# Performance work log

Measured on AMD Instinct MI355X. Metric: run time of the kernel, lower is better.

## Reference

```python
import jax, jax.numpy as jnp
import numpy as np

V, E, H = 50000, 300, 512
B, S = 64, 512


def setup_inputs() -> dict:
    key = jax.random.key(0)
    ks = jax.random.split(key, 10)
    sc = 1.0 / np.sqrt(H)
    return {
        "inputs": jax.random.randint(ks[0], (B, S), 0, V),
        "embed_table": jax.random.normal(ks[1], (V, E), jnp.float32),
        "W_ih_f": jax.random.normal(ks[2], (4 * H, E), jnp.float32) * sc,
        "W_hh_f": jax.random.normal(ks[3], (4 * H, H), jnp.float32) * sc,
        "b_ih_f": jax.random.normal(ks[4], (4 * H,), jnp.float32) * sc,
        "b_hh_f": jax.random.normal(ks[5], (4 * H,), jnp.float32) * sc,
        "W_ih_b": jax.random.normal(ks[6], (4 * H, E), jnp.float32) * sc,
        "W_hh_b": jax.random.normal(ks[7], (4 * H, H), jnp.float32) * sc,
        "b_ih_b": jax.random.normal(ks[8], (4 * H,), jnp.float32) * sc,
        "b_hh_b": jax.random.normal(ks[9], (4 * H,), jnp.float32) * sc,
    }


def _cell_from_gates(gates):
    # PyTorch LSTMCell gate order: i, f, g, o; here c_prev == 0 (faithful to source bug)
    i, f, g, o = jnp.split(gates, 4, axis=-1)
    c = jax.nn.sigmoid(i) * jnp.tanh(g)
    return jax.nn.sigmoid(o) * jnp.tanh(c)


def reference(inputs, embed_table, W_ih_f, W_hh_f, b_ih_f, b_hh_f,
              W_ih_b, W_hh_b, b_ih_b, b_hh_b):
    x = embed_table[inputs]  # [B,S,E]
    # 'forward LSTM': source always feeds (zero, zero) state -> no recurrence,
    # fully parallel over time. h contribution from W_hh is zero.
    gates_f = jnp.einsum('bse,ge->bsg', x, W_ih_f) + b_ih_f + b_hh_f  # [B,S,4H]
    h_f = _cell_from_gates(gates_f)  # [B,S,H]

    # backward LSTM: h carried across steps, c_prev always zero (faithful)
    x_gates_b = jnp.einsum('bse,ge->bsg', x, W_ih_b) + b_ih_b + b_hh_b  # [B,S,4H]
    xs = jnp.flip(x_gates_b, axis=1).transpose(1, 0, 2)  # [S,B,4H] reversed time

    def step(h, xt):
        h_new = _cell_from_gates(xt + h @ W_hh_b.T)
        return h_new, h_new

    h0 = jnp.zeros((x.shape[0], W_hh_b.shape[1]), x.dtype)
    _, hs_b = jax.lax.scan(step, h0, xs)  # [S,B,H], reversed time order
    h_b = jnp.flip(hs_b.transpose(1, 0, 2), axis=1)  # [B,S,H] original order

    concat = jnp.concatenate([h_f, h_b], axis=-1)  # [B,S,2H]
    return jnp.max(concat, axis=1)  # [B,2H]
```

## Files before the change

kernel.cpp:

```cpp
#include <hip/hip_runtime.h>
#include <cstdint>
#include <cstddef>

#define B_   64
#define S_   512
#define E_   300
#define EP   320
#define H_   512
#define G3   1536
#define CHUNKS 8
#define CHLEN  64
#define HALO   32
#define WPG    8

typedef float  f32x4 __attribute__((ext_vector_type(4)));
typedef short  s16x8 __attribute__((ext_vector_type(8)));
typedef unsigned long long u64;

__device__ __forceinline__ unsigned short f2bf(float f) {
  union { float f; unsigned u; } v; v.f = f;
  return (unsigned short)((v.u + 0x7fffu + ((v.u >> 16) & 1u)) >> 16);
}
__device__ __forceinline__ float bf2f(unsigned short s) {
  union { unsigned u; float f; } v; v.u = ((unsigned)s) << 16;
  return v.f;
}
__device__ __forceinline__ float sigm(float x) { return 1.0f / (1.0f + __expf(-x)); }
__device__ __forceinline__ float tanhf_(float x) { return 2.0f / (1.0f + __expf(-2.0f * x)) - 1.0f; }
__device__ __forceinline__ float cellh(float i, float g, float o) {
  float c = sigm(i) * tanhf_(g);
  return sigm(o) * tanhf_(c);
}

__device__ __forceinline__ float ldG(const float* p, long i) { return p[i]; }
__device__ __forceinline__ float ldG(const unsigned short* p, long i) { return bf2f(p[i]); }
__device__ __forceinline__ void stG(float* p, long i, float v) { p[i] = v; }
__device__ __forceinline__ void stG(unsigned short* p, long i, float v) { p[i] = f2bf(v); }
__device__ __forceinline__ void ld2G(const float* p, long i, float& a, float& b) {
  float2 t = *(const float2*)(p + i); a = t.x; b = t.y;
}
__device__ __forceinline__ void ld2G(const unsigned short* p, long i, float& a, float& b) {
  unsigned u = *(const unsigned*)(p + i);
  a = bf2f((unsigned short)(u & 0xffffu)); b = bf2f((unsigned short)(u >> 16));
}
__device__ __forceinline__ void ld4G(const float* p, long i, float4& v) {
  v = *(const float4*)(p + i);
}
__device__ __forceinline__ void ld4G(const unsigned short* p, long i, float4& v) {
  u64 u = *(const u64*)(p + i);
  v.x = bf2f((unsigned short)(u & 0xffffu));
  v.y = bf2f((unsigned short)((u >> 16) & 0xffffu));
  v.z = bf2f((unsigned short)((u >> 32) & 0xffffu));
  v.w = bf2f((unsigned short)(u >> 48));
}

__device__ __forceinline__ void bar_lgkm() {
  asm volatile("s_waitcnt lgkmcnt(0)\ns_barrier" ::: "memory");
}
__device__ __forceinline__ void bar_only() {
  asm volatile("s_barrier" ::: "memory");
}

__global__ __launch_bounds__(256)
void prep_kernel(const float* __restrict__ Wf, const float* __restrict__ Wb,
                 const float* __restrict__ bihf, const float* __restrict__ bhhf,
                 const float* __restrict__ bihb, const float* __restrict__ bhhb,
                 unsigned short* __restrict__ Wfp, unsigned short* __restrict__ Wbp,
                 float* __restrict__ bpf, float* __restrict__ bpb) {
  const int t0 = blockIdx.x * blockDim.x + threadIdx.x;
  const int stride = gridDim.x * blockDim.x;
  const int tot = G3 * EP;
  for (int idx = t0; idx < tot; idx += stride) {
    const int n = idx / EP, k = idx - n * EP;
    const int src = (n < H_) ? n : n + H_;
    const float vf = (k < E_) ? Wf[(size_t)src * E_ + k] : 0.0f;
    const float vb = (k < E_) ? Wb[(size_t)src * E_ + k] : 0.0f;
    Wfp[idx] = f2bf(vf);
    Wbp[idx] = f2bf(vb);
  }
  for (int n = t0; n < G3; n += stride) {
    const int src = (n < H_) ? n : n + H_;
    bpf[n] = bihf[src] + bhhf[src];
    bpb[n] = bihb[src] + bhhb[src];
  }
}

__global__ __launch_bounds__(256)
void xstage_kernel(const int* __restrict__ inp, const float* __restrict__ emb,
                   unsigned short* __restrict__ xbf) {
  const int t = blockIdx.x * blockDim.x + threadIdx.x;
  const int row = t / 80, q = t - row * 80;
  const int c0 = q * 4;
  const int vid = inp[row];
  unsigned short o[4];
#pragma unroll
  for (int e = 0; e < 4; ++e) {
    const int c = c0 + e;
    o[e] = (c < E_) ? f2bf(emb[(size_t)vid * E_ + c]) : (unsigned short)0;
  }
  uint2 pv;
  pv.x = (unsigned)o[0] | ((unsigned)o[1] << 16);
  pv.y = (unsigned)o[2] | ((unsigned)o[3] << 16);
  *(uint2*)&xbf[(size_t)row * EP + c0] = pv;
}

template<bool REMAP, typename GT>
__global__ __launch_bounds__(256)
void gemm_kernel(const unsigned short* __restrict__ A, const unsigned short* __restrict__ W,
                 const float* __restrict__ bias, GT* __restrict__ C) {
  __shared__ short lA[128 * 40];
  __shared__ short lB[128 * 40];
  const int tid = threadIdx.x;
  const int w = tid >> 6, l = tid & 63;
  const int wr = w >> 1, wc = w & 1;
  const int Mb = blockIdx.x * 128, Nb = blockIdx.y * 128;
  f32x4 acc[4][4];
#pragma unroll
  for (int i = 0; i < 4; ++i)
#pragma unroll
    for (int j = 0; j < 4; ++j) acc[i][j] = f32x4{0.f, 0.f, 0.f, 0.f};

  const int srow = tid >> 1, shalf = (tid & 1) * 16;
  for (int kk = 0; kk < EP; kk += 32) {
    const s16x8* ga = (const s16x8*)&A[(size_t)(Mb + srow) * EP + kk + shalf];
    const s16x8* gb = (const s16x8*)&W[(size_t)(Nb + srow) * EP + kk + shalf];
    s16x8 a0 = ga[0], a1 = ga[1], b0 = gb[0], b1 = gb[1];
    *(s16x8*)&lA[srow * 40 + shalf]     = a0;
    *(s16x8*)&lA[srow * 40 + shalf + 8] = a1;
    *(s16x8*)&lB[srow * 40 + shalf]     = b0;
    *(s16x8*)&lB[srow * 40 + shalf + 8] = b1;
    __syncthreads();
    s16x8 af[4], bf[4];
#pragma unroll
    for (int mt = 0; mt < 4; ++mt)
      af[mt] = *(const s16x8*)&lA[(wr * 64 + mt * 16 + (l & 15)) * 40 + 8 * (l >> 4)];
#pragma unroll
    for (int nt = 0; nt < 4; ++nt)
      bf[nt] = *(const s16x8*)&lB[(wc * 64 + nt * 16 + (l & 15)) * 40 + 8 * (l >> 4)];
#pragma unroll
    for (int mt = 0; mt < 4; ++mt)
#pragma unroll
      for (int nt = 0; nt < 4; ++nt)
        acc[mt][nt] = __builtin_amdgcn_mfma_f32_16x16x32_bf16(af[mt], bf[nt], acc[mt][nt], 0, 0, 0);
    __syncthreads();
  }
#pragma unroll
  for (int mt = 0; mt < 4; ++mt) {
#pragma unroll
    for (int nt = 0; nt < 4; ++nt) {
      const int gc = Nb + wc * 64 + nt * 16 + (l & 15);
      const float bv = bias[gc];
#pragma unroll
      for (int r = 0; r < 4; ++r) {
        const int gr = Mb + wr * 64 + mt * 16 + (l >> 4) * 4 + r;
        const int orow = REMAP ? (((gr & 511) << 6) | (gr >> 9)) : gr;
        stG(C, (long)orow * G3 + gc, acc[mt][nt][r] + bv);
      }
    }
  }
}

template<typename GT>
__global__ __launch_bounds__(256)
void cellmax1_kernel(const GT* __restrict__ G, float* __restrict__ part) {
  const int b = blockIdx.x, ch = blockIdx.y, tid = threadIdx.x;
  const int j0 = tid * 2;
  float mx0 = -2.f, mx1 = -2.f;
#pragma unroll 1
  for (int s = ch * 64; s < ch * 64 + 64; ++s) {
    const long base = (long)(b * S_ + s) * G3;
    float i0, i1, g0, g1, o0, o1;
    ld2G(G, base + j0, i0, i1);
    ld2G(G, base + 512 + j0, g0, g1);
    ld2G(G, base + 1024 + j0, o0, o1);
    mx0 = fmaxf(mx0, cellh(i0, g0, o0));
    mx1 = fmaxf(mx1, cellh(i1, g1, o1));
  }
  part[(ch * 64 + b) * 512 + j0]     = mx0;
  part[(ch * 64 + b) * 512 + j0 + 1] = mx1;
}

__global__ __launch_bounds__(256)
void cellmax2_kernel(const float* __restrict__ part, float* __restrict__ out) {
  const int b = blockIdx.x, tid = threadIdx.x;
  const int j0 = tid * 2;
  float mx0 = -2.f, mx1 = -2.f;
#pragma unroll
  for (int ch = 0; ch < 8; ++ch) {
    const float2 v = *(const float2*)&part[(ch * 64 + b) * 512 + j0];
    mx0 = fmaxf(mx0, v.x);
    mx1 = fmaxf(mx1, v.y);
  }
  out[b * 1024 + j0] = mx0;
  out[b * 1024 + j0 + 1] = mx1;
}

__global__ __launch_bounds__(256)
void breduce_kernel(const float* __restrict__ bpart, float* __restrict__ out) {
  const int b = blockIdx.x, tid = threadIdx.x;
  const int j0 = tid * 2;
  float mx0 = -2.f, mx1 = -2.f;
#pragma unroll
  for (int ch = 0; ch < CHUNKS; ++ch) {
    const float2 v = *(const float2*)&bpart[(ch * 64 + b) * 512 + j0];
    mx0 = fmaxf(mx0, v.x);
    mx1 = fmaxf(mx1, v.y);
  }
  out[b * 1024 + 512 + j0] = mx0;
  out[b * 1024 + 512 + j0 + 1] = mx1;
}

__global__ __launch_bounds__(256) void zero_sync_kernel(unsigned* p) {
  for (int i = threadIdx.x; i < 4096; i += 256) p[i] = 0;
}

template<typename GT>
__global__ __launch_bounds__(384, 1)
void scan_kernel(const float* __restrict__ Whh, const GT* __restrict__ Gb,
                 u64* __restrict__ hbuf, unsigned* __restrict__ flags,
                 float* __restrict__ bpart) {
  __shared__ __align__(16) unsigned hl[16 * 262];
  __shared__ float gbuf[12][16][20];

  const int tid = threadIdx.x;
  const int wv = tid >> 6, l = tid & 63;
  const int grp = blockIdx.x >> 3, rank = blockIdx.x & 7;
  const int ch = blockIdx.y;
  const int dom = grp * CHUNKS + ch;
  const int jbase = rank * 64;

  const int own_lo = ch * CHLEN, own_hi = own_lo + CHLEN;
  int ts = own_hi - 1 + HALO;
  if (ts > S_ - 1) ts = S_ - 1;

  const int tt0 = wv * 2, tt1 = tt0 + 1;
  s16x8 wf0[16], wf1[16];
  {
    const int nb0 = (tt0 >> 2) * 512 + jbase + (tt0 & 3) * 16 + (l & 15);
    const int nb1 = (tt1 >> 2) * 512 + jbase + (tt1 & 3) * 16 + (l & 15);
    const int s0 = (nb0 < 512) ? nb0 : nb0 + 512;
    const int s1 = (nb1 < 512) ? nb1 : nb1 + 512;
    const float* w0 = Whh + (size_t)s0 * 512 + 8 * (l >> 4);
    const float* w1 = Whh + (size_t)s1 * 512 + 8 * (l >> 4);
#pragma unroll
    for (int kc = 0; kc < 16; ++kc) {
      float4 a = *(const float4*)(w0 + kc * 32);
      float4 b = *(const float4*)(w0 + kc * 32 + 4);
      s16x8 v;
      v[0] = (short)f2bf(a.x); v[1] = (short)f2bf(a.y);
      v[2] = (short)f2bf(a.z); v[3] = (short)f2bf(a.w);
      v[4] = (short)f2bf(b.x); v[5] = (short)f2bf(b.y);
      v[6] = (short)f2bf(b.z); v[7] = (short)f2bf(b.w);
      wf0[kc] = v;
      a = *(const float4*)(w1 + kc * 32);
      b = *(const float4*)(w1 + kc * 32 + 4);
      v[0] = (short)f2bf(a.x); v[1] = (short)f2bf(a.y);
      v[2] = (short)f2bf(a.z); v[3] = (short)f2bf(a.w);
      v[4] = (short)f2bf(b.x); v[5] = (short)f2bf(b.y);
      v[6] = (short)f2bf(b.z); v[7] = (short)f2bf(b.w);
      wf1[kc] = v;
    }
  }

  const int mrow = (l >> 4) * 4;
  const int slot = tid - 64;
  const bool nl  = (slot >= 0 && slot < 256);
  const int prow = nl ? (slot >> 4) : 0;
  const int q    = slot & 15;
  const int tile = q >> 2, cit0 = (q & 3) * 4;
  const unsigned short* hls = (const unsigned short*)hl;
  float4 mx = {-2.f, -2.f, -2.f, -2.f};

  float4 xi = {0,0,0,0}, xg = {0,0,0,0}, xo = {0,0,0,0};
  if (nl) {
    const long rowb = (long)(ts * 64 + grp * 16 + prow) * G3 + (jbase + q * 4);
    ld4G(Gb, rowb, xi);
    ld4G(Gb, rowb + 512, xg);
    ld4G(Gb, rowb + 1024, xo);
  }

  __syncthreads();

#pragma unroll 1
  for (int t = ts; t >= own_lo; --t) {
    if (t != ts && wv == 0) {
      const unsigned seq = (unsigned)(ts - t);
      const unsigned* fp = flags + (unsigned)(dom * 8 + (l & 7)) * 16;
      unsigned mine = seq;
      for (int it = 0; it < (1 << 16); ++it) {
        if (l < 8) {
          unsigned v;
          asm volatile("global_load_dword %0, %1, off sc0 sc1\ns_waitcnt vmcnt(0)"
                       : "=v"(v) : "v"(fp) : "memory");
          mine = v;
        }
        if (__all((int)(mine >= seq))) break;
        __builtin_amdgcn_s_sleep(1);
      }
    }
    bar_only();

    if (t != ts && tid < 256) {
      const u64* hs = hbuf + (size_t)(((t + 1) & 1) * 32 + dom) * 2048 + tid;
      u64 v0, v1, v2, v3, v4, v5, v6, v7;
      asm volatile(
        "global_load_dwordx2 %0, %8, off sc0 sc1\n\t"
        "global_load_dwordx2 %1, %9, off sc0 sc1\n\t"
        "global_load_dwordx2 %2, %10, off sc0 sc1\n\t"
        "global_load_dwordx2 %3, %11, off sc0 sc1\n\t"
        "global_load_dwordx2 %4, %12, off sc0 sc1\n\t"
        "global_load_dwordx2 %5, %13, off sc0 sc1\n\t"
        "global_load_dwordx2 %6, %14, off sc0 sc1\n\t"
        "global_load_dwordx2 %7, %15, off sc0 sc1\n\t"
        "s_waitcnt vmcnt(0)"
        : "=&v"(v0), "=&v"(v1), "=&v"(v2), "=&v"(v3),
          "=&v"(v4), "=&v"(v5), "=&v"(v6), "=&v"(v7)
        : "v"(hs), "v"(hs + 256), "v"(hs + 512), "v"(hs + 768),
          "v"(hs + 1024), "v"(hs + 1280), "v"(hs + 1536), "v"(hs + 1792)
        : "memory");
      const int i0 = tid;
      *(u64*)&hl[((i0)        >> 7) * 262 + (((i0)        & 127) * 2)] = v0;
      *(u64*)&hl[((i0 + 256)  >> 7) * 262 + (((i0 + 256)  & 127) * 2)] = v1;
      *(u64*)&hl[((i0 + 512)  >> 7) * 262 + (((i0 + 512)  & 127) * 2)] = v2;
      *(u64*)&hl[((i0 + 768)  >> 7) * 262 + (((i0 + 768)  & 127) * 2)] = v3;
      *(u64*)&hl[((i0 + 1024) >> 7) * 262 + (((i0 + 1024) & 127) * 2)] = v4;
      *(u64*)&hl[((i0 + 1280) >> 7) * 262 + (((i0 + 1280) & 127) * 2)] = v5;
      *(u64*)&hl[((i0 + 1536) >> 7) * 262 + (((i0 + 1536) & 127) * 2)] = v6;
      *(u64*)&hl[((i0 + 1792) >> 7) * 262 + (((i0 + 1792) & 127) * 2)] = v7;
    }
    bar_lgkm();

    f32x4 a00 = {0,0,0,0}, a01 = {0,0,0,0}, a10 = {0,0,0,0}, a11 = {0,0,0,0};
    if (t != ts) {
#pragma unroll
      for (int kc = 0; kc < 16; kc += 2) {
        s16x8 f0 = *(const s16x8*)&hls[(l & 15) * 524 + (kc + 0) * 32 + 8 * (l >> 4)];
        s16x8 f1 = *(const s16x8*)&hls[(l & 15) * 524 + (kc + 1) * 32 + 8 * (l >> 4)];
        a00 = __builtin_amdgcn_mfma_f32_16x16x32_bf16(f0, wf0[kc + 0], a00, 0, 0, 0);
        a10 = __builtin_amdgcn_mfma_f32_16x16x32_bf16(f0, wf1[kc + 0], a10, 0, 0, 0);
        a01 = __builtin_amdgcn_mfma_f32_16x16x32_bf16(f1, wf0[kc + 1], a01, 0, 0, 0);
        a11 = __builtin_amdgcn_mfma_f32_16x16x32_bf16(f1, wf1[kc + 1], a11, 0, 0, 0);
      }
    }
#pragma unroll
    for (int r = 0; r < 4; ++r) {
      gbuf[tt0][mrow + r][l & 15] = a00[r] + a01[r];
      gbuf[tt1][mrow + r][l & 15] = a10[r] + a11[r];
    }
    bar_lgkm();

    if (nl) {
      float h[4];
#pragma unroll
      for (int cc = 0; cc < 4; ++cc) {
        const int cit = cit0 + cc;
        const float gi = gbuf[tile][prow][cit]     + ((const float*)&xi)[cc];
        const float gg = gbuf[4 + tile][prow][cit] + ((const float*)&xg)[cc];
        const float go = gbuf[8 + tile][prow][cit] + ((const float*)&xo)[cc];
        h[cc] = cellh(gi, gg, go);
      }
      if (t < own_hi) {
        mx.x = fmaxf(mx.x, h[0]); mx.y = fmaxf(mx.y, h[1]);
        mx.z = fmaxf(mx.z, h[2]); mx.w = fmaxf(mx.w, h[3]);
      }
      if (t > own_lo) {
        const u64 pk = (u64)((unsigned)f2bf(h[0]) | ((unsigned)f2bf(h[1]) << 16))
                     | ((u64)((unsigned)f2bf(h[2]) | ((unsigned)f2bf(h[3]) << 16)) << 32);
        u64* dst = hbuf + (size_t)((t & 1) * 32 + dom) * 2048
                        + prow * 128 + rank * 16 + q;
        asm volatile("global_store_dwordx2 %0, %1, off sc0 sc1" :: "v"(dst), "v"(pk) : "memory");
        const long rowb = (long)((t - 1) * 64 + grp * 16 + prow) * G3 + (jbase + q * 4);
        ld4G(Gb, rowb, xi);
        ld4G(Gb, rowb + 512, xg);
        ld4G(Gb, rowb + 1024, xo);
        asm volatile("s_waitcnt vmcnt(3)" ::: "memory");
      }
    }
    bar_only();
    if (t > own_lo && tid == 64) {
      unsigned* fp = &flags[(dom * 8 + rank) * 16];
      const unsigned sv = (unsigned)(ts - t + 1);
      asm volatile("global_atomic_swap %0, %1, off" :: "v"(fp), "v"(sv) : "memory");
    }
  }
  if (nl) {
    const int b = grp * 16 + prow;
    *(float4*)&bpart[(ch * 64 + b) * 512 + jbase + q * 4] = mx;
  }
}

extern "C" void kernel_launch(void* const* d_in, const int* in_sizes, int n_in,
                              void* d_out, int out_size, void* d_ws, size_t ws_size,
                              hipStream_t stream) {
  const int*   inp  = (const int*)  d_in[0];
  const float* emb  = (const float*)d_in[1];
  const float* Wihf = (const float*)d_in[2];
  const float* bihf = (const float*)d_in[4];
  const float* bhhf = (const float*)d_in[5];
  const float* Wihb = (const float*)d_in[6];
  const float* Whhb = (const float*)d_in[7];
  const float* bihb = (const float*)d_in[8];
  const float* bhhb = (const float*)d_in[9];
  float* out = (float*)d_out;
  char* ws = (char*)d_ws;

  const size_t o_xbf   = 0;
  const size_t o_Wfp   = o_xbf + 20971520;
  const size_t o_Wbp   = o_Wfp + 983040;
  const size_t o_bpf   = o_Wbp + 983040;
  const size_t o_bpb   = o_bpf + 6144;
  const size_t o_hbuf  = o_bpb + 6144;
  const size_t o_sync  = o_hbuf + 1048576;
  const size_t o_part  = o_sync + 32768;
  const size_t o_bpart = o_part + 1048576;
  const size_t o_G     = o_bpart + 1048576;
  const size_t need_f32 = o_G + (size_t)32768 * G3 * 4;

  unsigned short* xbf = (unsigned short*)(ws + o_xbf);
  unsigned short* Wfp = (unsigned short*)(ws + o_Wfp);
  unsigned short* Wbp = (unsigned short*)(ws + o_Wbp);
  float* bpf = (float*)(ws + o_bpf);
  float* bpb = (float*)(ws + o_bpb);
  u64* hbuf = (u64*)(ws + o_hbuf);
  unsigned* flags = (unsigned*)(ws + o_sync);
  float* part = (float*)(ws + o_part);
  float* bpart = (float*)(ws + o_bpart);
  void* G = (void*)(ws + o_G);

  hipLaunchKernelGGL(prep_kernel, dim3(512), dim3(256), 0, stream,
                     Wihf, Wihb, bihf, bhhf, bihb, bhhb, Wfp, Wbp, bpf, bpb);
  hipLaunchKernelGGL(xstage_kernel, dim3(10240), dim3(256), 0, stream, inp, emb, xbf);
  hipLaunchKernelGGL(zero_sync_kernel, dim3(1), dim3(256), 0, stream, flags);

  {
    unsigned short* Gf = (unsigned short*)G;
    hipLaunchKernelGGL((gemm_kernel<false, unsigned short>), dim3(256, 12), dim3(256), 0, stream,
                       xbf, Wfp, bpf, Gf);
    hipLaunchKernelGGL((cellmax1_kernel<unsigned short>), dim3(64, 8), dim3(256), 0, stream, Gf, part);
    hipLaunchKernelGGL(cellmax2_kernel, dim3(64), dim3(256), 0, stream, part, out);
  }
  if (ws_size >= need_f32) {
    float* Gbuf = (float*)G;
    hipLaunchKernelGGL((gemm_kernel<true, float>), dim3(256, 12), dim3(256), 0, stream,
                       xbf, Wbp, bpb, Gbuf);
    hipLaunchKernelGGL((scan_kernel<float>), dim3(32, CHUNKS), dim3(384), 0, stream,
                       Whhb, Gbuf, hbuf, flags, bpart);
  } else {
    unsigned short* Gbuf = (unsigned short*)G;
    hipLaunchKernelGGL((gemm_kernel<true, unsigned short>), dim3(256, 12), dim3(256), 0, stream,
                       xbf, Wbp, bpb, Gbuf);
    hipLaunchKernelGGL((scan_kernel<unsigned short>), dim3(32, CHUNKS), dim3(384), 0, stream,
                       Whhb, Gbuf, hbuf, flags, bpart);
  }
  hipLaunchKernelGGL(breduce_kernel, dim3(64), dim3(256), 0, stream, bpart, out);
}
```

Before: 788.2 us.

## Double scan time chunks, prepack Whh to bf16, use bf16 gates always

Splits the backward recurrence into 16 time chunks of 32 steps instead of 8 of 64, so twice as many workgroups run the scan in parallel with a shorter serial path. The cost is halo recomputation that now equals the owned chunk length. Whh is converted to bf16 once in the prep kernel instead of in every scan block. The hidden-state exchange now uses wider dwordx4 loads. The fp32 gate buffer path is dropped and bf16 gates are always used, which lowers memory traffic but changes numerics.

After: 918.5 us. +16.5%, slower.

```diff
diff --git a/kernel.cpp b/kernel.cpp
--- a/kernel.cpp
+++ b/kernel.cpp
@@ -8,8 +8,8 @@
 #define EP   320
 #define H_   512
 #define G3   1536
-#define CHUNKS 8
-#define CHLEN  64
+#define CHUNKS 16
+#define CHLEN  32
 #define HALO   32
 #define WPG    8
 
@@ -63,9 +63,11 @@
 
 __global__ __launch_bounds__(256)
 void prep_kernel(const float* __restrict__ Wf, const float* __restrict__ Wb,
+                 const float* __restrict__ Whh,
                  const float* __restrict__ bihf, const float* __restrict__ bhhf,
                  const float* __restrict__ bihb, const float* __restrict__ bhhb,
                  unsigned short* __restrict__ Wfp, unsigned short* __restrict__ Wbp,
+                 unsigned short* __restrict__ Whp,
                  float* __restrict__ bpf, float* __restrict__ bpb) {
   const int t0 = blockIdx.x * blockDim.x + threadIdx.x;
   const int stride = gridDim.x * blockDim.x;
@@ -77,6 +79,12 @@
     const float vb = (k < E_) ? Wb[(size_t)src * E_ + k] : 0.0f;
     Wfp[idx] = f2bf(vf);
     Wbp[idx] = f2bf(vb);
+  }
+  const int totw = G3 * H_;
+  for (int idx = t0; idx < totw; idx += stride) {
+    const int n = idx >> 9, k = idx & 511;
+    const int src = (n < H_) ? n : n + H_;
+    Whp[idx] = f2bf(Whh[(size_t)src * H_ + k]);
   }
   for (int n = t0; n < G3; n += stride) {
     const int src = (n < H_) ? n : n + H_;
@@ -211,12 +219,12 @@
 }
 
 __global__ __launch_bounds__(256) void zero_sync_kernel(unsigned* p) {
-  for (int i = threadIdx.x; i < 4096; i += 256) p[i] = 0;
+  for (int i = threadIdx.x; i < 8192; i += 256) p[i] = 0;
 }
 
 template<typename GT>
 __global__ __launch_bounds__(384, 1)
-void scan_kernel(const float* __restrict__ Whh, const GT* __restrict__ Gb,
+void scan_kernel(const unsigned short* __restrict__ Whp, const GT* __restrict__ Gb,
                  u64* __restrict__ hbuf, unsigned* __restrict__ flags,
                  float* __restrict__ bpart) {
   __shared__ __align__(16) unsigned hl[16 * 262];
@@ -234,32 +242,15 @@
   if (ts > S_ - 1) ts = S_ - 1;
 
   const int tt0 = wv * 2, tt1 = tt0 + 1;
+  const int nb0 = (tt0 >> 2) * 512 + jbase + (tt0 & 3) * 16 + (l & 15);
+  const int nb1 = (tt1 >> 2) * 512 + jbase + (tt1 & 3) * 16 + (l & 15);
+  const unsigned short* w0 = Whp + (size_t)nb0 * 512 + 8 * (l >> 4);
+  const unsigned short* w1 = Whp + (size_t)nb1 * 512 + 8 * (l >> 4);
   s16x8 wf0[16], wf1[16];
-  {
-    const int nb0 = (tt0 >> 2) * 512 + jbase + (tt0 & 3) * 16 + (l & 15);
-    const int nb1 = (tt1 >> 2) * 512 + jbase + (tt1 & 3) * 16 + (l & 15);
-    const int s0 = (nb0 < 512) ? nb0 : nb0 + 512;
-    const int s1 = (nb1 < 512) ? nb1 : nb1 + 512;
-    const float* w0 = Whh + (size_t)s0 * 512 + 8 * (l >> 4);
-    const float* w1 = Whh + (size_t)s1 * 512 + 8 * (l >> 4);
-#pragma unroll
-    for (int kc = 0; kc < 16; ++kc) {
-      float4 a = *(const float4*)(w0 + kc * 32);
-      float4 b = *(const float4*)(w0 + kc * 32 + 4);
-      s16x8 v;
-      v[0] = (short)f2bf(a.x); v[1] = (short)f2bf(a.y);
-      v[2] = (short)f2bf(a.z); v[3] = (short)f2bf(a.w);
-      v[4] = (short)f2bf(b.x); v[5] = (short)f2bf(b.y);
-      v[6] = (short)f2bf(b.z); v[7] = (short)f2bf(b.w);
-      wf0[kc] = v;
-      a = *(const float4*)(w1 + kc * 32);
-      b = *(const float4*)(w1 + kc * 32 + 4);
-      v[0] = (short)f2bf(a.x); v[1] = (short)f2bf(a.y);
-      v[2] = (short)f2bf(a.z); v[3] = (short)f2bf(a.w);
-      v[4] = (short)f2bf(b.x); v[5] = (short)f2bf(b.y);
-      v[6] = (short)f2bf(b.z); v[7] = (short)f2bf(b.w);
-      wf1[kc] = v;
-    }
+#pragma unroll
+  for (int kc = 0; kc < 16; ++kc) {
+    wf0[kc] = *(const s16x8*)(w0 + kc * 32);
+    wf1[kc] = *(const s16x8*)(w1 + kc * 32);
   }
 
   const int mrow = (l >> 4) * 4;
@@ -301,32 +292,29 @@
     bar_only();
 
     if (t != ts && tid < 256) {
-      const u64* hs = hbuf + (size_t)(((t + 1) & 1) * 32 + dom) * 2048 + tid;
-      u64 v0, v1, v2, v3, v4, v5, v6, v7;
+      const uint4* hs = (const uint4*)(hbuf + (size_t)(((t + 1) & 1) * 64 + dom) * 2048) + tid;
+      uint4 v0, v1, v2, v3;
       asm volatile(
-        "global_load_dwordx2 %0, %8, off sc0 sc1\n\t"
-        "global_load_dwordx2 %1, %9, off sc0 sc1\n\t"
-        "global_load_dwordx2 %2, %10, off sc0 sc1\n\t"
-        "global_load_dwordx2 %3, %11, off sc0 sc1\n\t"
-        "global_load_dwordx2 %4, %12, off sc0 sc1\n\t"
-        "global_load_dwordx2 %5, %13, off sc0 sc1\n\t"
-        "global_load_dwordx2 %6, %14, off sc0 sc1\n\t"
-        "global_load_dwordx2 %7, %15, off sc0 sc1\n\t"
+        "global_load_dwordx4 %0, %4, off sc0 sc1\n\t"
+        "global_load_dwordx4 %1, %5, off sc0 sc1\n\t"
+        "global_load_dwordx4 %2, %6, off sc0 sc1\n\t"
+        "global_load_dwordx4 %3, %7, off sc0 sc1\n\t"
         "s_waitcnt vmcnt(0)"
-        : "=&v"(v0), "=&v"(v1), "=&v"(v2), "=&v"(v3),
-          "=&v"(v4), "=&v"(v5), "=&v"(v6), "=&v"(v7)
-        : "v"(hs), "v"(hs + 256), "v"(hs + 512), "v"(hs + 768),
-          "v"(hs + 1024), "v"(hs + 1280), "v"(hs + 1536), "v"(hs + 1792)
+        : "=&v"(v0), "=&v"(v1), "=&v"(v2), "=&v"(v3)
+        : "v"(hs), "v"(hs + 256), "v"(hs + 512), "v"(hs + 768)
         : "memory");
-      const int i0 = tid;
-      *(u64*)&hl[((i0)        >> 7) * 262 + (((i0)        & 127) * 2)] = v0;
-      *(u64*)&hl[((i0 + 256)  >> 7) * 262 + (((i0 + 256)  & 127) * 2)] = v1;
-      *(u64*)&hl[((i0 + 512)  >> 7) * 262 + (((i0 + 512)  & 127) * 2)] = v2;
-      *(u64*)&hl[((i0 + 768)  >> 7) * 262 + (((i0 + 768)  & 127) * 2)] = v3;
-      *(u64*)&hl[((i0 + 1024) >> 7) * 262 + (((i0 + 1024) & 127) * 2)] = v4;
-      *(u64*)&hl[((i0 + 1280) >> 7) * 262 + (((i0 + 1280) & 127) * 2)] = v5;
-      *(u64*)&hl[((i0 + 1536) >> 7) * 262 + (((i0 + 1536) & 127) * 2)] = v6;
-      *(u64*)&hl[((i0 + 1792) >> 7) * 262 + (((i0 + 1792) & 127) * 2)] = v7;
+#define PUTQ(J, V) do {                                                    \
+        const int a0_ = 2 * (J), a1_ = a0_ + 1;                            \
+        *(u64*)&hl[(a0_ >> 7) * 262 + (a0_ & 127) * 2] =                   \
+            (u64)(V).x | ((u64)(V).y << 32);                               \
+        *(u64*)&hl[(a1_ >> 7) * 262 + (a1_ & 127) * 2] =                   \
+            (u64)(V).z | ((u64)(V).w << 32);                               \
+      } while (0)
+      PUTQ(tid, v0);
+      PUTQ(tid + 256, v1);
+      PUTQ(tid + 512, v2);
+      PUTQ(tid + 768, v3);
+#undef PUTQ
     }
     bar_lgkm();
 
@@ -366,7 +354,7 @@
       if (t > own_lo) {
         const u64 pk = (u64)((unsigned)f2bf(h[0]) | ((unsigned)f2bf(h[1]) << 16))
                      | ((u64)((unsigned)f2bf(h[2]) | ((unsigned)f2bf(h[3]) << 16)) << 32);
-        u64* dst = hbuf + (size_t)((t & 1) * 32 + dom) * 2048
+        u64* dst = hbuf + (size_t)((t & 1) * 64 + dom) * 2048
                         + prow * 128 + rank * 16 + q;
         asm volatile("global_store_dwordx2 %0, %1, off sc0 sc1" :: "v"(dst), "v"(pk) : "memory");
         const long rowb = (long)((t - 1) * 64 + grp * 16 + prow) * G3 + (jbase + q * 4);
@@ -407,50 +395,40 @@
   const size_t o_xbf   = 0;
   const size_t o_Wfp   = o_xbf + 20971520;
   const size_t o_Wbp   = o_Wfp + 983040;
-  const size_t o_bpf   = o_Wbp + 983040;
+  const size_t o_Whp   = o_Wbp + 983040;
+  const size_t o_bpf   = o_Whp + 1572864;
   const size_t o_bpb   = o_bpf + 6144;
   const size_t o_hbuf  = o_bpb + 6144;
-  const size_t o_sync  = o_hbuf + 1048576;
+  const size_t o_sync  = o_hbuf + 2097152;
   const size_t o_part  = o_sync + 32768;
   const size_t o_bpart = o_part + 1048576;
-  const size_t o_G     = o_bpart + 1048576;
-  const size_t need_f32 = o_G + (size_t)32768 * G3 * 4;
+  const size_t o_G     = o_bpart + 2097152;
 
   unsigned short* xbf = (unsigned short*)(ws + o_xbf);
   unsigned short* Wfp = (unsigned short*)(ws + o_Wfp);
   unsigned short* Wbp = (unsigned short*)(ws + o_Wbp);
+  unsigned short* Whp = (unsigned short*)(ws + o_Whp);
   float* bpf = (float*)(ws + o_bpf);
   float* bpb = (float*)(ws + o_bpb);
   u64* hbuf = (u64*)(ws + o_hbuf);
   unsigned* flags = (unsigned*)(ws + o_sync);
   float* part = (float*)(ws + o_part);
   float* bpart = (float*)(ws + o_bpart);
-  void* G = (void*)(ws + o_G);
+  unsigned short* G = (unsigned short*)(ws + o_G);
 
   hipLaunchKernelGGL(prep_kernel, dim3(512), dim3(256), 0, stream,
-                     Wihf, Wihb, bihf, bhhf, bihb, bhhb, Wfp, Wbp, bpf, bpb);
+                     Wihf, Wihb, Whhb, bihf, bhhf, bihb, bhhb, Wfp, Wbp, Whp, bpf, bpb);
   hipLaunchKernelGGL(xstage_kernel, dim3(10240), dim3(256), 0, stream, inp, emb, xbf);
   hipLaunchKernelGGL(zero_sync_kernel, dim3(1), dim3(256), 0, stream, flags);
 
-  {
-    unsigned short* Gf = (unsigned short*)G;
-    hipLaunchKernelGGL((gemm_kernel<false, unsigned short>), dim3(256, 12), dim3(256), 0, stream,
-                       xbf, Wfp, bpf, Gf);
-    hipLaunchKernelGGL((cellmax1_kernel<unsigned short>), dim3(64, 8), dim3(256), 0, stream, Gf, part);
-    hipLaunchKernelGGL(cellmax2_kernel, dim3(64), dim3(256), 0, stream, part, out);
-  }
-  if (ws_size >= need_f32) {
-    float* Gbuf = (float*)G;
-    hipLaunchKernelGGL((gemm_kernel<true, float>), dim3(256, 12), dim3(256), 0, stream,
-                       xbf, Wbp, bpb, Gbuf);
-    hipLaunchKernelGGL((scan_kernel<float>), dim3(32, CHUNKS), dim3(384), 0, stream,
-                       Whhb, Gbuf, hbuf, flags, bpart);
-  } else {
-    unsigned short* Gbuf = (unsigned short*)G;
-    hipLaunchKernelGGL((gemm_kernel<true, unsigned short>), dim3(256, 12), dim3(256), 0, stream,
-                       xbf, Wbp, bpb, Gbuf);
-    hipLaunchKernelGGL((scan_kernel<unsigned short>), dim3(32, CHUNKS), dim3(384), 0, stream,
-                       Whhb, Gbuf, hbuf, flags, bpart);
-  }
+  hipLaunchKernelGGL((gemm_kernel<false, unsigned short>), dim3(256, 12), dim3(256), 0, stream,
+                     xbf, Wfp, bpf, G);
+  hipLaunchKernelGGL((cellmax1_kernel<unsigned short>), dim3(64, 8), dim3(256), 0, stream, G, part);
+  hipLaunchKernelGGL(cellmax2_kernel, dim3(64), dim3(256), 0, stream, part, out);
+
+  hipLaunchKernelGGL((gemm_kernel<true, unsigned short>), dim3(256, 12), dim3(256), 0, stream,
+                     xbf, Wbp, bpb, G);
+  hipLaunchKernelGGL((scan_kernel<unsigned short>), dim3(32, CHUNKS), dim3(384), 0, stream,
+                     Whp, G, hbuf, flags, bpart);
   hipLaunchKernelGGL(breduce_kernel, dim3(64), dim3(256), 0, stream, bpart, out);
 }
```
